# Optimization experiments

Hardware: AMD Instinct MI355X
Metric: run time of the kernel (lower is better)

Reference implementation:

```python
import jax, jax.numpy as jnp
import numpy as np

DIM = 256; HEADS = 8; B = 8; N = 128; MLP_HID = 4 * DIM


def _ln(x, g, b):
    m = x.mean(-1, keepdims=True)
    v = ((x - m) ** 2).mean(-1, keepdims=True)
    return (x - m) / jnp.sqrt(v + 1e-5) * g + b


def _mlp(x, W1, b1, W2, b2):
    return jax.nn.relu(x @ W1 + b1) @ W2 + b2


def setup_inputs():
    key = jax.random.key(0)
    ks = iter(jax.random.split(key, 48))
    def p(*shape):
        return jax.random.normal(next(ks), shape, jnp.float32) * 0.02
    inp = {
        'x': jax.random.normal(next(ks), (B, N, DIM), jnp.float32),
        'y': jax.random.normal(next(ks), (B, N, N, DIM), jnp.float32),
        'heads': HEADS,
    }
    for nm in ['q', 'k', 'v', 'e', 'oe', 'on']:
        inp['W' + nm] = p(DIM, DIM)
        inp['b' + nm] = p(DIM)
    for nm in ['ln1', 'ln3', 'ln4', 'ln5', 'ln6']:
        inp[nm + '_g'] = jnp.ones((DIM,), jnp.float32)
        inp[nm + '_b'] = jnp.zeros((DIM,), jnp.float32)
    inp['m1_W1'] = p(DIM, MLP_HID); inp['m1_b1'] = p(MLP_HID)
    inp['m1_W2'] = p(MLP_HID, DIM); inp['m1_b2'] = p(DIM)
    inp['m2_W1'] = p(DIM, MLP_HID); inp['m2_b1'] = p(MLP_HID)
    inp['m2_W2'] = p(MLP_HID, DIM); inp['m2_b2'] = p(DIM)
    return inp


def reference(x, y, heads, Wq, bq, Wk, bk, Wv, bv, We, be, Woe, boe, Won, bon,
              ln1_g, ln1_b, ln3_g, ln3_b, ln4_g, ln4_b, ln5_g, ln5_b, ln6_g, ln6_b,
              m1_W1, m1_b1, m1_W2, m1_b2, m2_W1, m2_b1, m2_W2, m2_b2):
    b, n, c = x.shape
    dk = c // heads
    x1 = _ln(x, ln1_g, ln1_b)
    q = (x1 @ Wq + bq).reshape(b, n, heads, dk)
    k = (x1 @ Wk + bk).reshape(b, n, heads, dk)
    v = (x1 @ Wv + bv).reshape(b, n, heads, dk)
    e = (y @ We + be).reshape(b, n, n, heads, dk)
    # elementwise QK (not a dot product), edge-modulated: (b,n,n,h,dk)
    attn = (q[:, :, None] * k[:, None]) / jnp.sqrt(jnp.float32(dk))
    attn = attn * (e + 1.0) * e
    edge = attn.reshape(b, n, n, c) @ Woe + boe
    attn = jax.nn.softmax(attn, axis=2)  # softmax over key/node axis
    node = (attn * v[:, None]).sum(axis=2).reshape(b, n, c)
    node = node @ Won + bon
    x2 = _ln(x1 + node, ln3_g, ln3_b)
    y2 = _ln(edge + y, ln4_g, ln4_b)
    x_out = _ln(x2 + _mlp(x2, m1_W1, m1_b1, m1_W2, m1_b2), ln5_g, ln5_b)
    y_out = _ln(y2 + _mlp(y2, m2_W1, m2_b1, m2_W2, m2_b2), ln6_g, ln6_b)
    return (x_out, y_out)
```

## Files before the change

kernel.cpp:

```cpp
#include <hip/hip_runtime.h>
#include <hip/hip_bf16.h>


#define DIMC 256
#define NSEQ 128
#define NB 8
#define HID 1024
#define EROWS (NB * NSEQ * NSEQ)

typedef __attribute__((ext_vector_type(8)))  short short8;
typedef __attribute__((ext_vector_type(16))) float f32x16;

__device__ __forceinline__ short f2bf(float f) {
    union { float f; unsigned u; } v; v.f = f;
    unsigned r = (v.u + 0x7FFF + ((v.u >> 16) & 1)) >> 16;
    return (short)r;
}
__device__ __forceinline__ float bf2f(short s) {
    union { unsigned u; float f; } v; v.u = ((unsigned)(unsigned short)s) << 16;
    return v.f;
}

__device__ __forceinline__ float wave_sum(float v) {
    #pragma unroll
    for (int o = 32; o; o >>= 1) v += __shfl_xor(v, o, 64);
    return v;
}

__device__ __forceinline__ float block_reduce_sum(float v, float* sc, int t) {
    #pragma unroll
    for (int o = 32; o > 0; o >>= 1) v += __shfl_down(v, o, 64);
    __syncthreads();
    if ((t & 63) == 0) sc[t >> 6] = v;
    __syncthreads();
    return sc[0] + sc[1] + sc[2] + sc[3];
}

__global__ __launch_bounds__(256, 2) void k_ln_qkv(
    const float* __restrict__ X, const float* __restrict__ g, const float* __restrict__ be,
    const float* __restrict__ Wq, const float* __restrict__ bq,
    const float* __restrict__ Wk, const float* __restrict__ bk,
    const float* __restrict__ Wv, const float* __restrict__ bv,
    float* __restrict__ X1, float* __restrict__ Q, float* __restrict__ K, float* __restrict__ V)
{
    __shared__ float xs[DIMC];
    __shared__ float red[4];
    const int t = threadIdx.x;
    const int row = blockIdx.x;
    float v = X[(size_t)row * DIMC + t];
    float mu = block_reduce_sum(v, red, t) * (1.f / DIMC);
    float d = v - mu;
    float var = block_reduce_sum(d * d, red, t) * (1.f / DIMC);
    float x1v = d * rsqrtf(var + 1e-5f) * g[t] + be[t];
    xs[t] = x1v;
    X1[(size_t)row * DIMC + t] = x1v;
    __syncthreads();
    float aq = bq[t], ak = bk[t], av = bv[t];
    #pragma unroll 4
    for (int k2 = 0; k2 < DIMC; ++k2) {
        float xv = xs[k2];
        aq = fmaf(xv, Wq[k2 * DIMC + t], aq);
        ak = fmaf(xv, Wk[k2 * DIMC + t], ak);
        av = fmaf(xv, Wv[k2 * DIMC + t], av);
    }
    Q[(size_t)row * DIMC + t] = aq;
    K[(size_t)row * DIMC + t] = ak;
    V[(size_t)row * DIMC + t] = av;
}

__global__ __launch_bounds__(256) void k_transpose_bf16(
    const float* __restrict__ src, short* __restrict__ dst, int M, int N)
{
    __shared__ short tile[32][33];
    const int t = threadIdx.x, tx = t & 31, ty = t >> 5;
    const int bx = blockIdx.x, by = blockIdx.y;
    #pragma unroll
    for (int r = ty; r < 32; r += 8)
        tile[r][tx] = f2bf(src[(size_t)(by * 32 + r) * N + bx * 32 + tx]);
    __syncthreads();
    #pragma unroll
    for (int r = ty; r < 32; r += 8)
        dst[(size_t)(bx * 32 + r) * M + by * 32 + tx] = tile[tx][r];
}

__global__ __launch_bounds__(256, 2) void k_e_attn_m(
    const float* __restrict__ Y, const short* __restrict__ WeT,
    const float* __restrict__ be,
    const float* __restrict__ Q, const float* __restrict__ Kp,
    short* __restrict__ ATTb)
{
    __shared__ __align__(16) short As[64][256];
    const int t = threadIdx.x, w = t >> 6, lane = t & 63;
    const int l31 = lane & 31, kg = lane >> 5;
    const size_t R0 = (size_t)blockIdx.x * 64;

    for (int r = w * 16; r < w * 16 + 16; ++r) {
        float4 y4 = *(const float4*)&Y[(R0 + r) * DIMC + lane * 4];
        short4 s4;
        s4.x = f2bf(y4.x); s4.y = f2bf(y4.y); s4.z = f2bf(y4.z); s4.w = f2bf(y4.w);
        *(short4*)&As[r][(((lane >> 1) ^ (r & 7)) << 3) + (lane & 1) * 4] = s4;
    }
    __syncthreads();

    const int rh = (w & 1) * 32, cbase = (w >> 1) * 128;
    const int sw = l31 & 7;
    f32x16 acc[4];
    #pragma unroll
    for (int a = 0; a < 4; ++a)
        #pragma unroll
        for (int i = 0; i < 16; ++i) acc[a][i] = 0.f;

    #pragma unroll
    for (int ks = 0; ks < 16; ++ks) {
        const int gk = 2 * ks + kg;
        short8 a = *(const short8*)&As[rh + l31][(gk ^ sw) * 8];
        #pragma unroll
        for (int tt = 0; tt < 4; ++tt) {
            short8 b = *(const short8*)&WeT[(size_t)(cbase + tt * 32 + l31) * DIMC + gk * 8];
            acc[tt] = __builtin_amdgcn_mfma_f32_32x32x16_bf16(a, b, acc[tt], 0, 0, 0);
        }
    }

    const int m0 = (int)(R0);
    const int qrow = m0 >> 7, bidx = m0 >> 14, jb = m0 & 127;
    const float isq = 0.17677669529663687f;
    #pragma unroll
    for (int tt = 0; tt < 4; ++tt) {
        const int n = cbase + tt * 32 + l31;
        const float qv = Q[(size_t)qrow * DIMC + n];
        const float bb = be[n];
        #pragma unroll
        for (int i = 0; i < 16; ++i) {
            const int row = rh + 4 * kg + (i & 3) + 8 * (i >> 2);
            const float kv = Kp[(size_t)((bidx << 7) + jb + row) * DIMC + n];
            const float e = acc[tt][i] + bb;
            const float qk = qv * kv * isq;
            ATTb[(size_t)(m0 + row) * DIMC + n] = f2bf(qk * (e + 1.f) * e);
        }
    }
}

__global__ __launch_bounds__(256, 2) void k_edge_m(
    const short* __restrict__ ATTb, const short* __restrict__ WoeT,
    const float* __restrict__ boe, float* __restrict__ EDGE)
{
    __shared__ __align__(16) short As[64][256];
    const int t = threadIdx.x, w = t >> 6, lane = t & 63;
    const int l31 = lane & 31, kg = lane >> 5;
    const size_t R0 = (size_t)blockIdx.x * 64;

    #pragma unroll
    for (int it = 0; it < 8; ++it) {
        const int r = w * 16 + it * 2 + kg;
        short8 v = *(const short8*)&ATTb[(R0 + r) * DIMC + l31 * 8];
        *(short8*)&As[r][((l31 ^ (r & 7))) * 8] = v;
    }
    __syncthreads();

    const int rh = (w & 1) * 32, cbase = (w >> 1) * 128;
    const int sw = l31 & 7;
    f32x16 acc[4];
    #pragma unroll
    for (int a = 0; a < 4; ++a)
        #pragma unroll
        for (int i = 0; i < 16; ++i) acc[a][i] = 0.f;

    #pragma unroll
    for (int ks = 0; ks < 16; ++ks) {
        const int gk = 2 * ks + kg;
        short8 a = *(const short8*)&As[rh + l31][(gk ^ sw) * 8];
        #pragma unroll
        for (int tt = 0; tt < 4; ++tt) {
            short8 b = *(const short8*)&WoeT[(size_t)(cbase + tt * 32 + l31) * DIMC + gk * 8];
            acc[tt] = __builtin_amdgcn_mfma_f32_32x32x16_bf16(a, b, acc[tt], 0, 0, 0);
        }
    }

    const int m0 = (int)(R0);
    #pragma unroll
    for (int tt = 0; tt < 4; ++tt) {
        const int n = cbase + tt * 32 + l31;
        const float bb = boe[n];
        #pragma unroll
        for (int i = 0; i < 16; ++i) {
            const int row = rh + 4 * kg + (i & 3) + 8 * (i >> 2);
            EDGE[(size_t)(m0 + row) * DIMC + n] = acc[tt][i] + bb;
        }
    }
}

__global__ __launch_bounds__(256, 2) void k_node_x(
    const short* __restrict__ ATTb, const float* __restrict__ V,
    const float* __restrict__ X1,
    const float* __restrict__ Won, const float* __restrict__ bon,
    const float* __restrict__ g3, const float* __restrict__ b3,
    const float* __restrict__ W1, const float* __restrict__ b1,
    const float* __restrict__ W2, const float* __restrict__ b2,
    const float* __restrict__ g5, const float* __restrict__ b5,
    float* __restrict__ OUTX)
{
    __shared__ float ns[DIMC];
    __shared__ float x2s[DIMC];
    __shared__ float hs[HID];
    __shared__ float red[4];
    const int t = threadIdx.x;
    const int bi = blockIdx.x;
    const int b = bi >> 7;
    const short* arow = ATTb + (size_t)bi * NSEQ * DIMC + t;
    const float* vbase = V + (size_t)b * NSEQ * DIMC + t;
    float mx = -3.4e38f, l = 0.f, acc = 0.f;
    for (int j = 0; j < NSEQ; ++j) {
        float a = bf2f(arow[(size_t)j * DIMC]);
        float vv = vbase[(size_t)j * DIMC];
        if (a > mx) { float sc = __expf(mx - a); l *= sc; acc *= sc; mx = a; }
        float p = __expf(a - mx);
        l += p;
        acc = fmaf(p, vv, acc);
    }
    ns[t] = acc / l;
    __syncthreads();
    float o = bon[t];
    #pragma unroll 4
    for (int k2 = 0; k2 < DIMC; ++k2) o = fmaf(ns[k2], Won[k2 * DIMC + t], o);
    float resid = X1[(size_t)bi * DIMC + t] + o;
    float mu = block_reduce_sum(resid, red, t) * (1.f / DIMC);
    float d = resid - mu;
    float var = block_reduce_sum(d * d, red, t) * (1.f / DIMC);
    float x2 = d * rsqrtf(var + 1e-5f) * g3[t] + b3[t];
    x2s[t] = x2;
    __syncthreads();
    float4 h = *(const float4*)&b1[t * 4];
    for (int k2 = 0; k2 < DIMC; ++k2) {
        float xv = x2s[k2];
        float4 w = *(const float4*)&W1[(size_t)k2 * HID + t * 4];
        h.x = fmaf(xv, w.x, h.x); h.y = fmaf(xv, w.y, h.y);
        h.z = fmaf(xv, w.z, h.z); h.w = fmaf(xv, w.w, h.w);
    }
    h.x = fmaxf(h.x, 0.f); h.y = fmaxf(h.y, 0.f); h.z = fmaxf(h.z, 0.f); h.w = fmaxf(h.w, 0.f);
    *(float4*)&hs[t * 4] = h;
    __syncthreads();
    float o2 = b2[t];
    #pragma unroll 4
    for (int hh = 0; hh < HID; ++hh) o2 = fmaf(hs[hh], W2[(size_t)hh * DIMC + t], o2);
    float r2 = x2 + o2;
    float mu2 = block_reduce_sum(r2, red, t) * (1.f / DIMC);
    float d2 = r2 - mu2;
    float v2 = block_reduce_sum(d2 * d2, red, t) * (1.f / DIMC);
    OUTX[(size_t)bi * DIMC + t] = d2 * rsqrtf(v2 + 1e-5f) * g5[t] + b5[t];
}

__global__ __launch_bounds__(256, 2) void k_mlp_y3(
    float* __restrict__ EY, const float* __restrict__ Y,
    const float* __restrict__ g4, const float* __restrict__ b4,
    const short* __restrict__ W1T, const float* __restrict__ b1,
    const short* __restrict__ W2T, const float* __restrict__ b2,
    const float* __restrict__ g6, const float* __restrict__ b6)
{
    __shared__ __align__(16) short As[64][256];
    __shared__ __align__(16) short Hs[2][64][64];
    const int t = threadIdx.x;
    const int w = t >> 6, lane = t & 63;
    const int l31 = lane & 31, kg = lane >> 5;
    const size_t R0 = (size_t)blockIdx.x * 64;

    {
        const float4 gv = *(const float4*)&g4[lane * 4];
        const float4 bv = *(const float4*)&b4[lane * 4];
        const int gk = lane >> 1;
        for (int r = w * 16; r < w * 16 + 16; ++r) {
            const float4 e4 = *(const float4*)&EY[(R0 + r) * DIMC + lane * 4];
            const float4 y4 = *(const float4*)&Y[(R0 + r) * DIMC + lane * 4];
            float v0 = e4.x + y4.x, v1 = e4.y + y4.y, v2 = e4.z + y4.z, v3 = e4.w + y4.w;
            float mu = wave_sum(v0 + v1 + v2 + v3) * (1.f / DIMC);
            float d0 = v0 - mu, d1 = v1 - mu, d2 = v2 - mu, d3 = v3 - mu;
            float var = wave_sum(d0 * d0 + d1 * d1 + d2 * d2 + d3 * d3) * (1.f / DIMC);
            float rs = rsqrtf(var + 1e-5f);
            short* p = &As[r][(gk ^ (r & 7)) * 8 + (lane & 1) * 4];
            short4 s4;
            s4.x = f2bf(d0 * rs * gv.x + bv.x);
            s4.y = f2bf(d1 * rs * gv.y + bv.y);
            s4.z = f2bf(d2 * rs * gv.z + bv.z);
            s4.w = f2bf(d3 * rs * gv.w + bv.w);
            *(short4*)p = s4;
        }
    }
    __syncthreads();

    const int tr1 = w & 1, tc1 = w >> 1;
    const int arow1 = tr1 * 32 + l31;
    const int a1sw = l31 & 7;
    const int r7 = l31 & 7;
    const int hcol = tc1 * 32 + l31;

    f32x16 acc2[4];
    #pragma unroll
    for (int a = 0; a < 4; ++a)
        #pragma unroll
        for (int i = 0; i < 16; ++i) acc2[a][i] = 0.f;

    const short* w2p0 = &W2T[(size_t)((2 * w + 0) * 32 + l31) * HID];
    const short* w2p1 = &W2T[(size_t)((2 * w + 1) * 32 + l31) * HID];

    auto gemm1 = [&](int h) {
        const short* w1p = &W1T[(size_t)(h * 64 + hcol) * DIMC];
        f32x16 c1a, c1b;
        #pragma unroll
        for (int i = 0; i < 16; ++i) { c1a[i] = 0.f; c1b[i] = 0.f; }
        #pragma unroll
        for (int ks = 0; ks < 8; ++ks) {
            const int gk = 2 * ks + kg;
            short8 a = *(const short8*)&As[arow1][(gk ^ a1sw) * 8];
            short8 b = *(const short8*)&w1p[gk * 8];
            c1a = __builtin_amdgcn_mfma_f32_32x32x16_bf16(a, b, c1a, 0, 0, 0);
        }
        #pragma unroll
        for (int ks = 8; ks < 16; ++ks) {
            const int gk = 2 * ks + kg;
            short8 a = *(const short8*)&As[arow1][(gk ^ a1sw) * 8];
            short8 b = *(const short8*)&w1p[gk * 8];
            c1b = __builtin_amdgcn_mfma_f32_32x32x16_bf16(a, b, c1b, 0, 0, 0);
        }
        const float bb = b1[h * 64 + hcol];
        short (*Hw)[64] = Hs[h & 1];
        #pragma unroll
        for (int i = 0; i < 16; ++i) {
            const int row = tr1 * 32 + 4 * kg + (i & 3) + 8 * (i >> 2);
            Hw[row][(((hcol >> 3) ^ (row & 7)) << 3) + (hcol & 7)] =
                f2bf(fmaxf(c1a[i] + c1b[i] + bb, 0.f));
        }
    };
    auto gemm2 = [&](int h) {
        const short (*Hr)[64] = Hs[h & 1];
        #pragma unroll
        for (int ks = 0; ks < 4; ++ks) {
            const int gk = 2 * ks + kg;
            short8 a0 = *(const short8*)&Hr[l31][(gk ^ r7) * 8];
            short8 a1 = *(const short8*)&Hr[32 + l31][(gk ^ r7) * 8];
            const size_t kglob = (size_t)h * 64 + ks * 16 + kg * 8;
            short8 b0 = *(const short8*)&w2p0[kglob];
            short8 b1v = *(const short8*)&w2p1[kglob];
            acc2[0] = __builtin_amdgcn_mfma_f32_32x32x16_bf16(a0, b0,  acc2[0], 0, 0, 0);
            acc2[1] = __builtin_amdgcn_mfma_f32_32x32x16_bf16(a0, b1v, acc2[1], 0, 0, 0);
            acc2[2] = __builtin_amdgcn_mfma_f32_32x32x16_bf16(a1, b0,  acc2[2], 0, 0, 0);
            acc2[3] = __builtin_amdgcn_mfma_f32_32x32x16_bf16(a1, b1v, acc2[3], 0, 0, 0);
        }
    };

    gemm1(0);
    __syncthreads();
    for (int h = 1; h < 16; ++h) {
        gemm2(h - 1);
        gemm1(h);
        __syncthreads();
    }
    gemm2(15);

    #pragma unroll
    for (int a = 0; a < 4; ++a) {
        const int tr = a >> 1, tc2 = 2 * w + (a & 1);
        const int col = tc2 * 32 + l31;
        const float bb = b2[col];
        #pragma unroll
        for (int i = 0; i < 16; ++i) {
            const int row = tr * 32 + 4 * kg + (i & 3) + 8 * (i >> 2);
            const int phys = ((col >> 3) ^ (row & 7)) * 8 + (col & 7);
            As[row][phys] = f2bf(bf2f(As[row][phys]) + acc2[a][i] + bb);
        }
    }
    __syncthreads();

    {
        const float4 gv = *(const float4*)&g6[lane * 4];
        const float4 bv = *(const float4*)&b6[lane * 4];
        const int gk = lane >> 1;
        for (int r = w * 16; r < w * 16 + 16; ++r) {
            const short4 s4 = *(const short4*)&As[r][(gk ^ (r & 7)) * 8 + (lane & 1) * 4];
            float v0 = bf2f(s4.x), v1 = bf2f(s4.y), v2 = bf2f(s4.z), v3 = bf2f(s4.w);
            float mu = wave_sum(v0 + v1 + v2 + v3) * (1.f / DIMC);
            float d0 = v0 - mu, d1 = v1 - mu, d2 = v2 - mu, d3 = v3 - mu;
            float var = wave_sum(d0 * d0 + d1 * d1 + d2 * d2 + d3 * d3) * (1.f / DIMC);
            float rs = rsqrtf(var + 1e-5f);
            float4 o;
            o.x = d0 * rs * gv.x + bv.x;
            o.y = d1 * rs * gv.y + bv.y;
            o.z = d2 * rs * gv.z + bv.z;
            o.w = d3 * rs * gv.w + bv.w;
            *(float4*)&EY[(R0 + r) * DIMC + lane * 4] = o;
        }
    }
}

extern "C" void kernel_launch(void* const* d_in, const int* in_sizes, int n_in,
                              void* d_out, int out_size, void* d_ws, size_t ws_size,
                              hipStream_t stream) {
    const float* x    = (const float*)d_in[0];
    const float* y    = (const float*)d_in[1];
    const float* Wq   = (const float*)d_in[3];  const float* bq  = (const float*)d_in[4];
    const float* Wk   = (const float*)d_in[5];  const float* bk  = (const float*)d_in[6];
    const float* Wv   = (const float*)d_in[7];  const float* bv  = (const float*)d_in[8];
    const float* We   = (const float*)d_in[9];  const float* be  = (const float*)d_in[10];
    const float* Woe  = (const float*)d_in[11]; const float* boe = (const float*)d_in[12];
    const float* Won  = (const float*)d_in[13]; const float* bon = (const float*)d_in[14];
    const float* ln1g = (const float*)d_in[15]; const float* ln1b = (const float*)d_in[16];
    const float* ln3g = (const float*)d_in[17]; const float* ln3b = (const float*)d_in[18];
    const float* ln4g = (const float*)d_in[19]; const float* ln4b = (const float*)d_in[20];
    const float* ln5g = (const float*)d_in[21]; const float* ln5b = (const float*)d_in[22];
    const float* ln6g = (const float*)d_in[23]; const float* ln6b = (const float*)d_in[24];
    const float* m1W1 = (const float*)d_in[25]; const float* m1b1 = (const float*)d_in[26];
    const float* m1W2 = (const float*)d_in[27]; const float* m1b2 = (const float*)d_in[28];
    const float* m2W1 = (const float*)d_in[29]; const float* m2b1 = (const float*)d_in[30];
    const float* m2W2 = (const float*)d_in[31]; const float* m2b2 = (const float*)d_in[32];

    float* outx = (float*)d_out;
    float* outy = (float*)d_out + NB * NSEQ * DIMC;

    float* ws  = (float*)d_ws;
    float* X1  = ws;
    float* Q   = ws + 262144;
    float* K   = ws + 524288;
    float* V   = ws + 786432;
    short* wsS = (short*)(ws + 1048576);
    short* WeT  = wsS;
    short* WoeT = wsS + 65536;
    short* W1T  = wsS + 131072;
    short* W2T  = wsS + 393216;
    short* ATTb = wsS + 655360;

    k_transpose_bf16<<<dim3(8, 8),  256, 0, stream>>>(We,   WeT,  DIMC, DIMC);
    k_transpose_bf16<<<dim3(8, 8),  256, 0, stream>>>(Woe,  WoeT, DIMC, DIMC);
    k_transpose_bf16<<<dim3(32, 8), 256, 0, stream>>>(m2W1, W1T,  DIMC, HID);
    k_transpose_bf16<<<dim3(8, 32), 256, 0, stream>>>(m2W2, W2T,  HID,  DIMC);

    k_ln_qkv<<<NB * NSEQ, 256, 0, stream>>>(x, ln1g, ln1b, Wq, bq, Wk, bk, Wv, bv, X1, Q, K, V);
    k_e_attn_m<<<EROWS / 64, 256, 0, stream>>>(y, WeT, be, Q, K, ATTb);
    k_edge_m<<<EROWS / 64, 256, 0, stream>>>(ATTb, WoeT, boe, outy);
    k_node_x<<<NB * NSEQ, 256, 0, stream>>>(ATTb, V, X1, Won, bon, ln3g, ln3b,
                                            m1W1, m1b1, m1W2, m1b2, ln5g, ln5b, outx);
    k_mlp_y3<<<EROWS / 64, 256, 0, stream>>>(outy, y, ln4g, ln4b,
                                             W1T, m2b1, W2T, m2b2, ln6g, ln6b);
}
```

Measured before the change: 1.132 ms.

## Restructure edge MLP to stream packed weight chunks through LDS with 16x16 MFMA

Rewrites the edge-path MLP kernel so each 512-thread block handles 128 rows. Each wave keeps its 16-row A fragments in registers, while combined W1/W2 64-column chunks are prefetched from global memory and double-buffered in LDS. A new prep kernel packs both weights into a swizzled bf16 layout per hidden chunk. The final residual and LayerNorm are done directly on the accumulators with shuffle reductions. The aim is to cut the repeated global weight reads per block and the per-step syncs, at the cost of 128KB of LDS, which limits occupancy, and heavy register pressure.

```diff
diff --git a/kernel.cpp b/kernel.cpp
--- a/kernel.cpp
+++ b/kernel.cpp
@@ -10,6 +10,7 @@
 
 typedef __attribute__((ext_vector_type(8)))  short short8;
 typedef __attribute__((ext_vector_type(16))) float f32x16;
+typedef __attribute__((ext_vector_type(4)))  float f32x4;
 
 __device__ __forceinline__ short f2bf(float f) {
     union { float f; unsigned u; } v; v.f = f;
@@ -81,6 +82,24 @@
     #pragma unroll
     for (int r = ty; r < 32; r += 8)
         dst[(size_t)(bx * 32 + r) * M + by * 32 + tx] = tile[tx][r];
+}
+
+__global__ __launch_bounds__(256) void k_prep_wc(
+    const float* __restrict__ W1, const float* __restrict__ W2, short* __restrict__ Wc)
+{
+    const int h = blockIdx.x, t = threadIdx.x;
+    short* dst = Wc + (size_t)h * 32768;
+    const int hh = t & 63, kq = t >> 6;
+    for (int k0 = 0; k0 < 256; k0 += 4) {
+        const int k = k0 + kq;
+        float v = W1[(size_t)k * HID + h * 64 + hh];
+        dst[hh * 256 + (((k >> 3) ^ (hh & 7)) << 3) + (k & 7)] = f2bf(v);
+    }
+    short* dst2 = dst + 16384;
+    for (int kk = 0; kk < 64; ++kk) {
+        float v = W2[(size_t)(h * 64 + kk) * DIMC + t];
+        dst2[t * 64 + (((kk >> 3) ^ (t & 7)) << 3) + (kk & 7)] = f2bf(v);
+    }
 }
 
 __global__ __launch_bounds__(256, 2) void k_e_attn_m(
@@ -249,25 +268,27 @@
     OUTX[(size_t)bi * DIMC + t] = d2 * rsqrtf(v2 + 1e-5f) * g5[t] + b5[t];
 }
 
-__global__ __launch_bounds__(256, 2) void k_mlp_y3(
+__global__ __launch_bounds__(512, 2) void k_mlp_y4(
     float* __restrict__ EY, const float* __restrict__ Y,
     const float* __restrict__ g4, const float* __restrict__ b4,
-    const short* __restrict__ W1T, const float* __restrict__ b1,
-    const short* __restrict__ W2T, const float* __restrict__ b2,
+    const short* __restrict__ Wc, const float* __restrict__ b1v,
+    const float* __restrict__ b2v,
     const float* __restrict__ g6, const float* __restrict__ b6)
 {
-    __shared__ __align__(16) short As[64][256];
-    __shared__ __align__(16) short Hs[2][64][64];
+    __shared__ __align__(16) short Wbuf[2][32768];
+    __shared__ __align__(16) short Hscr[8][16][72];
     const int t = threadIdx.x;
     const int w = t >> 6, lane = t & 63;
-    const int l31 = lane & 31, kg = lane >> 5;
-    const size_t R0 = (size_t)blockIdx.x * 64;
+    const int l15 = lane & 15, l4 = lane >> 4;
+    const int r7 = l15 & 7;
+    const size_t R0 = (size_t)blockIdx.x * 128;
 
     {
         const float4 gv = *(const float4*)&g4[lane * 4];
         const float4 bv = *(const float4*)&b4[lane * 4];
         const int gk = lane >> 1;
-        for (int r = w * 16; r < w * 16 + 16; ++r) {
+        for (int rr = 0; rr < 16; ++rr) {
+            const int r = w * 16 + rr;
             const float4 e4 = *(const float4*)&EY[(R0 + r) * DIMC + lane * 4];
             const float4 y4 = *(const float4*)&Y[(R0 + r) * DIMC + lane * 4];
             float v0 = e4.x + y4.x, v1 = e4.y + y4.y, v2 = e4.z + y4.z, v3 = e4.w + y4.w;
@@ -275,117 +296,142 @@
             float d0 = v0 - mu, d1 = v1 - mu, d2 = v2 - mu, d3 = v3 - mu;
             float var = wave_sum(d0 * d0 + d1 * d1 + d2 * d2 + d3 * d3) * (1.f / DIMC);
             float rs = rsqrtf(var + 1e-5f);
-            short* p = &As[r][(gk ^ (r & 7)) * 8 + (lane & 1) * 4];
             short4 s4;
             s4.x = f2bf(d0 * rs * gv.x + bv.x);
             s4.y = f2bf(d1 * rs * gv.y + bv.y);
             s4.z = f2bf(d2 * rs * gv.z + bv.z);
             s4.w = f2bf(d3 * rs * gv.w + bv.w);
-            *(short4*)p = s4;
-        }
-    }
-    __syncthreads();
-
-    const int tr1 = w & 1, tc1 = w >> 1;
-    const int arow1 = tr1 * 32 + l31;
-    const int a1sw = l31 & 7;
-    const int r7 = l31 & 7;
-    const int hcol = tc1 * 32 + l31;
-
-    f32x16 acc2[4];
-    #pragma unroll
-    for (int a = 0; a < 4; ++a)
-        #pragma unroll
-        for (int i = 0; i < 16; ++i) acc2[a][i] = 0.f;
-
-    const short* w2p0 = &W2T[(size_t)((2 * w + 0) * 32 + l31) * HID];
-    const short* w2p1 = &W2T[(size_t)((2 * w + 1) * 32 + l31) * HID];
-
-    auto gemm1 = [&](int h) {
-        const short* w1p = &W1T[(size_t)(h * 64 + hcol) * DIMC];
-        f32x16 c1a, c1b;
-        #pragma unroll
-        for (int i = 0; i < 16; ++i) { c1a[i] = 0.f; c1b[i] = 0.f; }
-        #pragma unroll
-        for (int ks = 0; ks < 8; ++ks) {
-            const int gk = 2 * ks + kg;
-            short8 a = *(const short8*)&As[arow1][(gk ^ a1sw) * 8];
-            short8 b = *(const short8*)&w1p[gk * 8];
-            c1a = __builtin_amdgcn_mfma_f32_32x32x16_bf16(a, b, c1a, 0, 0, 0);
-        }
-        #pragma unroll
-        for (int ks = 8; ks < 16; ++ks) {
-            const int gk = 2 * ks + kg;
-            short8 a = *(const short8*)&As[arow1][(gk ^ a1sw) * 8];
-            short8 b = *(const short8*)&w1p[gk * 8];
-            c1b = __builtin_amdgcn_mfma_f32_32x32x16_bf16(a, b, c1b, 0, 0, 0);
-        }
-        const float bb = b1[h * 64 + hcol];
-        short (*Hw)[64] = Hs[h & 1];
-        #pragma unroll
-        for (int i = 0; i < 16; ++i) {
-            const int row = tr1 * 32 + 4 * kg + (i & 3) + 8 * (i >> 2);
-            Hw[row][(((hcol >> 3) ^ (row & 7)) << 3) + (hcol & 7)] =
-                f2bf(fmaxf(c1a[i] + c1b[i] + bb, 0.f));
-        }
-    };
-    auto gemm2 = [&](int h) {
-        const short (*Hr)[64] = Hs[h & 1];
-        #pragma unroll
-        for (int ks = 0; ks < 4; ++ks) {
-            const int gk = 2 * ks + kg;
-            short8 a0 = *(const short8*)&Hr[l31][(gk ^ r7) * 8];
-            short8 a1 = *(const short8*)&Hr[32 + l31][(gk ^ r7) * 8];
-            const size_t kglob = (size_t)h * 64 + ks * 16 + kg * 8;
-            short8 b0 = *(const short8*)&w2p0[kglob];
-            short8 b1v = *(const short8*)&w2p1[kglob];
-            acc2[0] = __builtin_amdgcn_mfma_f32_32x32x16_bf16(a0, b0,  acc2[0], 0, 0, 0);
-            acc2[1] = __builtin_amdgcn_mfma_f32_32x32x16_bf16(a0, b1v, acc2[1], 0, 0, 0);
-            acc2[2] = __builtin_amdgcn_mfma_f32_32x32x16_bf16(a1, b0,  acc2[2], 0, 0, 0);
-            acc2[3] = __builtin_amdgcn_mfma_f32_32x32x16_bf16(a1, b1v, acc2[3], 0, 0, 0);
-        }
-    };
-
-    gemm1(0);
-    __syncthreads();
-    for (int h = 1; h < 16; ++h) {
-        gemm2(h - 1);
-        gemm1(h);
+            *(short4*)&Wbuf[0][r * 256 + ((gk ^ (rr & 7)) << 3) + (lane & 1) * 4] = s4;
+        }
+    }
+
+    short8 af[8];
+    {
+        const int row = w * 16 + l15;
+        #pragma unroll
+        for (int kt = 0; kt < 8; ++kt)
+            af[kt] = *(const short8*)&Wbuf[0][row * 256 + (((kt * 4 + l4) ^ r7) << 3)];
+    }
+
+    {
+        #pragma unroll
+        for (int p = 0; p < 8; ++p) {
+            short8 v = *(const short8*)&Wc[p * 4096 + t * 8];
+            *(short8*)&Wbuf[1][p * 4096 + t * 8] = v;
+        }
+    }
+    __syncthreads();
+
+    f32x4 acc[16];
+    #pragma unroll
+    for (int i = 0; i < 16; ++i)
+        #pragma unroll
+        for (int j = 0; j < 4; ++j) acc[i][j] = 0.f;
+
+    for (int h = 0; h < 16; ++h) {
+        const short* Wlds = Wbuf[1 - (h & 1)];
+        short8 pf[8];
+        if (h < 15) {
+            const short* src = Wc + (size_t)(h + 1) * 32768;
+            #pragma unroll
+            for (int p = 0; p < 8; ++p) pf[p] = *(const short8*)&src[p * 4096 + t * 8];
+        }
+
+        f32x4 c1[4];
+        #pragma unroll
+        for (int i = 0; i < 4; ++i)
+            #pragma unroll
+            for (int j = 0; j < 4; ++j) c1[i][j] = 0.f;
+        #pragma unroll
+        for (int kt = 0; kt < 8; ++kt) {
+            const int gsw = ((kt * 4 + l4) ^ r7) << 3;
+            #pragma unroll
+            for (int tt = 0; tt < 4; ++tt) {
+                short8 b = *(const short8*)&Wlds[(tt * 16 + l15) * 256 + gsw];
+                c1[tt] = __builtin_amdgcn_mfma_f32_16x16x32_bf16(af[kt], b, c1[tt], 0, 0, 0);
+            }
+        }
+        #pragma unroll
+        for (int tt = 0; tt < 4; ++tt) {
+            const float bb = b1v[h * 64 + tt * 16 + l15];
+            #pragma unroll
+            for (int j = 0; j < 4; ++j)
+                Hscr[w][l4 * 4 + j][tt * 16 + l15] = f2bf(fmaxf(c1[tt][j] + bb, 0.f));
+        }
+        #pragma unroll
+        for (int kt2 = 0; kt2 < 2; ++kt2) {
+            short8 hf = *(const short8*)&Hscr[w][l15][kt2 * 32 + l4 * 8];
+            const int gsw2 = ((kt2 * 4 + l4) ^ r7) << 3;
+            #pragma unroll
+            for (int ct = 0; ct < 16; ++ct) {
+                short8 b = *(const short8*)&Wlds[16384 + (ct * 16 + l15) * 64 + gsw2];
+                acc[ct] = __builtin_amdgcn_mfma_f32_16x16x32_bf16(hf, b, acc[ct], 0, 0, 0);
+            }
+        }
+        if (h < 15) {
+            short* dst = Wbuf[h & 1];
+            #pragma unroll
+            for (int p = 0; p < 8; ++p) *(short8*)&dst[p * 4096 + t * 8] = pf[p];
+        }
         __syncthreads();
     }
-    gemm2(15);
-
-    #pragma unroll
-    for (int a = 0; a < 4; ++a) {
-        const int tr = a >> 1, tc2 = 2 * w + (a & 1);
-        const int col = tc2 * 32 + l31;
-        const float bb = b2[col];
-        #pragma unroll
-        for (int i = 0; i < 16; ++i) {
-            const int row = tr * 32 + 4 * kg + (i & 3) + 8 * (i >> 2);
-            const int phys = ((col >> 3) ^ (row & 7)) * 8 + (col & 7);
-            As[row][phys] = f2bf(bf2f(As[row][phys]) + acc2[a][i] + bb);
-        }
-    }
-    __syncthreads();
 
     {
-        const float4 gv = *(const float4*)&g6[lane * 4];
-        const float4 bv = *(const float4*)&b6[lane * 4];
-        const int gk = lane >> 1;
-        for (int r = w * 16; r < w * 16 + 16; ++r) {
-            const short4 s4 = *(const short4*)&As[r][(gk ^ (r & 7)) * 8 + (lane & 1) * 4];
-            float v0 = bf2f(s4.x), v1 = bf2f(s4.y), v2 = bf2f(s4.z), v3 = bf2f(s4.w);
-            float mu = wave_sum(v0 + v1 + v2 + v3) * (1.f / DIMC);
-            float d0 = v0 - mu, d1 = v1 - mu, d2 = v2 - mu, d3 = v3 - mu;
-            float var = wave_sum(d0 * d0 + d1 * d1 + d2 * d2 + d3 * d3) * (1.f / DIMC);
-            float rs = rsqrtf(var + 1e-5f);
-            float4 o;
-            o.x = d0 * rs * gv.x + bv.x;
-            o.y = d1 * rs * gv.y + bv.y;
-            o.z = d2 * rs * gv.z + bv.z;
-            o.w = d3 * rs * gv.w + bv.w;
-            *(float4*)&EY[(R0 + r) * DIMC + lane * 4] = o;
+        const int row = w * 16 + l15;
+        #pragma unroll
+        for (int kt = 0; kt < 8; ++kt)
+            *(short8*)&Wbuf[0][row * 256 + (((kt * 4 + l4) ^ r7) << 3)] = af[kt];
+    }
+    #pragma unroll
+    for (int ct = 0; ct < 16; ++ct) {
+        const int col = ct * 16 + l15;
+        const float bb = b2v[col];
+        const int gl = col >> 3;
+        #pragma unroll
+        for (int j = 0; j < 4; ++j) {
+            const int rloc = l4 * 4 + j;
+            short yv = Wbuf[0][(w * 16 + rloc) * 256 + ((gl ^ (rloc & 7)) << 3) + (col & 7)];
+            acc[ct][j] += bb + bf2f(yv);
+        }
+    }
+    float sx = 0.f, sy = 0.f, sz = 0.f, sw2 = 0.f;
+    #pragma unroll
+    for (int ct = 0; ct < 16; ++ct) {
+        sx += acc[ct][0]; sy += acc[ct][1]; sz += acc[ct][2]; sw2 += acc[ct][3];
+    }
+    #pragma unroll
+    for (int m = 1; m < 16; m <<= 1) {
+        sx += __shfl_xor(sx, m, 64); sy += __shfl_xor(sy, m, 64);
+        sz += __shfl_xor(sz, m, 64); sw2 += __shfl_xor(sw2, m, 64);
+    }
+    const float mu0 = sx * (1.f / DIMC), mu1 = sy * (1.f / DIMC);
+    const float mu2 = sz * (1.f / DIMC), mu3 = sw2 * (1.f / DIMC);
+    float vx = 0.f, vy = 0.f, vz = 0.f, vw = 0.f;
+    #pragma unroll
+    for (int ct = 0; ct < 16; ++ct) {
+        float d0 = acc[ct][0] - mu0, d1 = acc[ct][1] - mu1;
+        float d2 = acc[ct][2] - mu2, d3 = acc[ct][3] - mu3;
+        vx += d0 * d0; vy += d1 * d1; vz += d2 * d2; vw += d3 * d3;
+    }
+    #pragma unroll
+    for (int m = 1; m < 16; m <<= 1) {
+        vx += __shfl_xor(vx, m, 64); vy += __shfl_xor(vy, m, 64);
+        vz += __shfl_xor(vz, m, 64); vw += __shfl_xor(vw, m, 64);
+    }
+    const float rs0 = rsqrtf(vx * (1.f / DIMC) + 1e-5f);
+    const float rs1 = rsqrtf(vy * (1.f / DIMC) + 1e-5f);
+    const float rs2 = rsqrtf(vz * (1.f / DIMC) + 1e-5f);
+    const float rs3 = rsqrtf(vw * (1.f / DIMC) + 1e-5f);
+    #pragma unroll
+    for (int ct = 0; ct < 16; ++ct) {
+        const int col = ct * 16 + l15;
+        const float gg = g6[col], bo = b6[col];
+        #pragma unroll
+        for (int j = 0; j < 4; ++j) {
+            const float mj = (j == 0) ? mu0 : (j == 1) ? mu1 : (j == 2) ? mu2 : mu3;
+            const float rj = (j == 0) ? rs0 : (j == 1) ? rs1 : (j == 2) ? rs2 : rs3;
+            const int r = w * 16 + l4 * 4 + j;
+            EY[(R0 + r) * DIMC + col] = (acc[ct][j] - mj) * rj * gg + bo;
         }
     }
 }
@@ -422,20 +468,18 @@
     short* wsS = (short*)(ws + 1048576);
     short* WeT  = wsS;
     short* WoeT = wsS + 65536;
-    short* W1T  = wsS + 131072;
-    short* W2T  = wsS + 393216;
+    short* Wc   = wsS + 131072;
     short* ATTb = wsS + 655360;
 
     k_transpose_bf16<<<dim3(8, 8),  256, 0, stream>>>(We,   WeT,  DIMC, DIMC);
     k_transpose_bf16<<<dim3(8, 8),  256, 0, stream>>>(Woe,  WoeT, DIMC, DIMC);
-    k_transpose_bf16<<<dim3(32, 8), 256, 0, stream>>>(m2W1, W1T,  DIMC, HID);
-    k_transpose_bf16<<<dim3(8, 32), 256, 0, stream>>>(m2W2, W2T,  HID,  DIMC);
+    k_prep_wc<<<16, 256, 0, stream>>>(m2W1, m2W2, Wc);
 
     k_ln_qkv<<<NB * NSEQ, 256, 0, stream>>>(x, ln1g, ln1b, Wq, bq, Wk, bk, Wv, bv, X1, Q, K, V);
     k_e_attn_m<<<EROWS / 64, 256, 0, stream>>>(y, WeT, be, Q, K, ATTb);
     k_edge_m<<<EROWS / 64, 256, 0, stream>>>(ATTb, WoeT, boe, outy);
     k_node_x<<<NB * NSEQ, 256, 0, stream>>>(ATTb, V, X1, Won, bon, ln3g, ln3b,
                                             m1W1, m1b1, m1W2, m1b2, ln5g, ln5b, outx);
-    k_mlp_y3<<<EROWS / 64, 256, 0, stream>>>(outy, y, ln4g, ln4b,
-                                             W1T, m2b1, W2T, m2b2, ln6g, ln6b);
-}
+    k_mlp_y4<<<EROWS / 128, 512, 0, stream>>>(outy, y, ln4g, ln4b,
+                                              Wc, m2b1, m2b2, ln6g, ln6b);
+}
```

Measured after the change: 969.0 us. 1.17x faster.
